# Optimization experiments

Hardware: AMD Instinct MI355X
Metric: run time of the kernel (lower is better)

Reference implementation:

```python
import jax, jax.numpy as jnp
import numpy as np

N_NODES = 100000
DIM = 64
N_EDGES = 1250000
NR_LAYERS = 1
EPS = 1e-12  # F.normalize default eps


def setup_inputs() -> dict:
    key = jax.random.key(0)
    k1, k2, k3 = jax.random.split(key, 3)
    x = jax.random.normal(k1, (N_NODES, DIM), dtype=jnp.float32)
    edge_index = jax.random.randint(k2, (2, N_EDGES), 0, N_NODES, dtype=jnp.int64 if jax.config.jax_enable_x64 else jnp.int32)
    edge_weights = jax.random.uniform(k3, (N_EDGES, 1), dtype=jnp.float32)
    return {"x": x, "edge_index": edge_index, "edge_weights": edge_weights}


def _scatter_mean(x, src, dst, n_nodes):
    # gather source features along edges, mean-reduce onto destination nodes
    sums = jax.ops.segment_sum(x[src], dst, num_segments=n_nodes)  # [N, D]
    cnt = jax.ops.segment_sum(jnp.ones((src.shape[0],), x.dtype), dst, num_segments=n_nodes)
    return sums / jnp.maximum(cnt, 1.0)[:, None]


def _layer(x, src, dst):
    # Faithful to source: update() overwrites the linear output with
    # F.normalize(aggr_out); out_f == out_b since new_edge_index == edge_index.
    agg = _scatter_mean(x, src, dst, x.shape[0])  # [N, D]
    norm = jnp.linalg.norm(agg, axis=1, keepdims=True)
    h = agg / jnp.maximum(norm, EPS)
    return 2.0 * h  # out_f + out_b


def reference(x, edge_index, edge_weights):
    src = edge_index[0]
    dst = edge_index[1]
    for _ in range(NR_LAYERS):
        x = _layer(x, src, dst)
        x = jax.nn.relu(x)
    return x
```

## Files before the change

kernel.cpp:

```cpp
#include <hip/hip_runtime.h>

#define N_NODES 100000
#define DIM 64
#define N_EDGES 1250000
#define EPS 1e-12f

#define PART 128
#define NP ((N_NODES + PART - 1) / PART)
#define SLOT 2048
#define CSTRIDE 16
#define CH 4096
#define NCH ((N_EDGES + CH - 1) / CH)
#define BT 1024
#define EPT (CH / BT)

typedef unsigned short ushort8 __attribute__((ext_vector_type(8)));

__device__ inline unsigned short f2bf(float f) {
    unsigned int u = __float_as_uint(f);
    return (unsigned short)((u + 0x7FFFu + ((u >> 16) & 1u)) >> 16);
}
__device__ inline float bf2f(unsigned short h) {
    return __uint_as_float(((unsigned int)h) << 16);
}

__global__ void convert_kernel(const float4* __restrict__ x4,
                               ushort8* __restrict__ xh8) {
    int i = blockIdx.x * blockDim.x + threadIdx.x;
    if (i < N_NODES * DIM / 8) {
        float4 a = x4[2 * i];
        float4 b = x4[2 * i + 1];
        ushort8 o;
        o[0] = f2bf(a.x); o[1] = f2bf(a.y); o[2] = f2bf(a.z); o[3] = f2bf(a.w);
        o[4] = f2bf(b.x); o[5] = f2bf(b.y); o[6] = f2bf(b.z); o[7] = f2bf(b.w);
        xh8[i] = o;
    }
}

__global__ __launch_bounds__(BT)
void bucket_kernel(const int* __restrict__ src,
                   const int* __restrict__ dst,
                   int* __restrict__ pcursor,
                   int* __restrict__ ebuf) {
    __shared__ int hist[NP];
    __shared__ int lstart[NP];
    __shared__ int cur[NP];
    __shared__ int gb[NP];
    __shared__ int sorted[CH];
    int t = threadIdx.x;
    int e0 = blockIdx.x * CH;

    for (int p = t; p < NP; p += BT) hist[p] = 0;
    __syncthreads();

    int d[EPT];
    #pragma unroll
    for (int i = 0; i < EPT; ++i) {
        int e = e0 + i * BT + t;
        d[i] = (e < N_EDGES) ? dst[e] : -1;
        if (d[i] >= 0) atomicAdd(&hist[d[i] >> 7], 1);
    }
    __syncthreads();

    for (int p = t; p < NP; p += BT) {
        int c = hist[p];
        gb[p] = c ? atomicAdd(&pcursor[p * CSTRIDE], c) : 0;
    }
    for (int p = t; p < NP; p += BT) cur[p] = hist[p];
    __syncthreads();
    for (int off = 1; off < NP; off <<= 1) {
        int v = 0;
        if (t < NP) { v = cur[t]; if (t >= off) v += cur[t - off]; }
        __syncthreads();
        if (t < NP) cur[t] = v;
        __syncthreads();
    }
    if (t < NP) lstart[t] = (t > 0) ? cur[t - 1] : 0;
    __syncthreads();
    if (t < NP) cur[t] = lstart[t];
    __syncthreads();

    #pragma unroll
    for (int i = 0; i < EPT; ++i) {
        if (d[i] >= 0) {
            int e = e0 + i * BT + t;
            int p = d[i] >> 7;
            int pos = atomicAdd(&cur[p], 1);
            sorted[pos] = (src[e] << 7) | (d[i] & 127);
        }
    }
    __syncthreads();

    int wave = t >> 6, lane = t & 63;
    for (int p = wave; p < NP; p += (BT / 64)) {
        int c = hist[p];
        int base = p * SLOT + gb[p];
        int ls = lstart[p];
        for (int off = lane; off < c; off += 64)
            ebuf[base + off] = sorted[ls + off];
    }
}

__global__ __launch_bounds__(1024, 8)
void aggregate_kernel(const ushort8* __restrict__ xh8,
                      const int* __restrict__ pcursor,
                      const int* __restrict__ ebuf,
                      float* __restrict__ out) {
    __shared__ int lraw[SLOT];
    __shared__ int lcsr[SLOT];
    __shared__ int lhist[PART];
    __shared__ int lcur[PART];
    int p = blockIdx.x;
    int t = threadIdx.x;
    int wave = t >> 6, lane = t & 63;
    int n = lane >> 3;
    int sub = lane & 7;

    if (t < PART) lhist[t] = 0;
    __syncthreads();

    int cnt = pcursor[p * CSTRIDE];
    const int* __restrict__ eb = ebuf + p * SLOT;
    for (int i = t; i < cnt; i += 1024) {
        int pk = eb[i];
        lraw[i] = pk;
        atomicAdd(&lhist[pk & 127], 1);
    }
    __syncthreads();

    for (int off = 1; off < PART; off <<= 1) {
        int v = 0;
        if (t < PART) { v = lhist[t]; if (t >= off) v += lhist[t - off]; }
        __syncthreads();
        if (t < PART) lhist[t] = v;
        __syncthreads();
    }
    if (t < PART) lcur[t] = (t > 0) ? lhist[t - 1] : 0;
    __syncthreads();

    for (int i = t; i < cnt; i += 1024) {
        int pk = lraw[i];
        int pos = atomicAdd(&lcur[pk & 127], 1);
        lcsr[pos] = pk >> 7;
    }
    __syncthreads();

    int nl = wave * 8 + n;
    int gnode = p * PART + nl;
    int beg = nl ? lhist[nl - 1] : 0;
    int dn  = lhist[nl] - beg;

    float acc[8] = {0.f,0.f,0.f,0.f,0.f,0.f,0.f,0.f};
    for (int e = 0; e < dn; e += 4) {
        #pragma unroll
        for (int i = 0; i < 4; ++i) {
            if (e + i < dn) {
                int s = lcsr[beg + e + i];
                ushort8 v = xh8[(size_t)s * 8 + sub];
                #pragma unroll
                for (int k = 0; k < 8; ++k) acc[k] += bf2f(v[k]);
            }
        }
    }

    float ss = 0.f;
    #pragma unroll
    for (int k = 0; k < 8; ++k) ss += acc[k] * acc[k];
    ss += __shfl_xor(ss, 1, 64);
    ss += __shfl_xor(ss, 2, 64);
    ss += __shfl_xor(ss, 4, 64);

    float scale = 2.0f / fmaxf(sqrtf(ss), EPS);
    if (gnode < N_NODES) {
        float4 o0, o1;
        o0.x = fmaxf(acc[0] * scale, 0.f); o0.y = fmaxf(acc[1] * scale, 0.f);
        o0.z = fmaxf(acc[2] * scale, 0.f); o0.w = fmaxf(acc[3] * scale, 0.f);
        o1.x = fmaxf(acc[4] * scale, 0.f); o1.y = fmaxf(acc[5] * scale, 0.f);
        o1.z = fmaxf(acc[6] * scale, 0.f); o1.w = fmaxf(acc[7] * scale, 0.f);
        ((float4*)out)[(size_t)gnode * 16 + 2 * sub]     = o0;
        ((float4*)out)[(size_t)gnode * 16 + 2 * sub + 1] = o1;
    }
}

extern "C" void kernel_launch(void* const* d_in, const int* in_sizes, int n_in,
                              void* d_out, int out_size, void* d_ws, size_t ws_size,
                              hipStream_t stream) {
    const float* x  = (const float*)d_in[0];
    const int*   ei = (const int*)d_in[1];
    float* out = (float*)d_out;

    const int* src = ei;
    const int* dst = ei + N_EDGES;

    ushort8* xh  = (ushort8*)d_ws;
    int* pcursor = (int*)((char*)d_ws + (size_t)N_NODES * DIM * 2);
    int* ebuf    = pcursor + NP * CSTRIDE;

    hipMemsetAsync(pcursor, 0, NP * CSTRIDE * sizeof(int), stream);

    int cvb = (N_NODES * DIM / 8 + 255) / 256;
    convert_kernel<<<cvb, 256, 0, stream>>>((const float4*)x, xh);

    bucket_kernel<<<NCH, BT, 0, stream>>>(src, dst, pcursor, ebuf);

    aggregate_kernel<<<NP, 1024, 0, stream>>>(xh, pcursor, ebuf, out);
}
```

Before: 150.3 us.

## Fuse convert into bucket kernel, use wave-shuffle scans, halve block size

Merges the bf16 conversion kernel and the edge-bucketing kernel into one launch, with extra blocks doing the conversion. Replaces the shared-memory Hillis-Steele scans, which needed many barriers, with wave-level shuffle scans in both kernels. Block size drops from 1024 to 512, so the aggregation kernel handles two node groups per thread. The bucket scatter becomes a flat per-edge loop that uses a stored partition id instead of a per-partition wave loop. This removes one launch and many barriers, at the cost of extra LDS for the partition-id array and less parallelism per block.

Result: faster. 132.8 us (-11.6%).

```diff
diff --git a/kernel.cpp b/kernel.cpp
--- a/kernel.cpp
+++ b/kernel.cpp
@@ -11,8 +11,9 @@
 #define CSTRIDE 16
 #define CH 4096
 #define NCH ((N_EDGES + CH - 1) / CH)
-#define BT 1024
+#define BT 512
 #define EPT (CH / BT)
+#define NCV ((N_NODES * DIM / 8 + BT - 1) / BT)
 
 typedef unsigned short ushort8 __attribute__((ext_vector_type(8)));
 
@@ -24,32 +25,37 @@
     return __uint_as_float(((unsigned int)h) << 16);
 }
 
-__global__ void convert_kernel(const float4* __restrict__ x4,
-                               ushort8* __restrict__ xh8) {
-    int i = blockIdx.x * blockDim.x + threadIdx.x;
-    if (i < N_NODES * DIM / 8) {
-        float4 a = x4[2 * i];
-        float4 b = x4[2 * i + 1];
-        ushort8 o;
-        o[0] = f2bf(a.x); o[1] = f2bf(a.y); o[2] = f2bf(a.z); o[3] = f2bf(a.w);
-        o[4] = f2bf(b.x); o[5] = f2bf(b.y); o[6] = f2bf(b.z); o[7] = f2bf(b.w);
-        xh8[i] = o;
-    }
-}
-
 __global__ __launch_bounds__(BT)
-void bucket_kernel(const int* __restrict__ src,
-                   const int* __restrict__ dst,
-                   int* __restrict__ pcursor,
-                   int* __restrict__ ebuf) {
+void convert_bucket_kernel(const float4* __restrict__ x4,
+                           ushort8* __restrict__ xh8,
+                           const int* __restrict__ src,
+                           const int* __restrict__ dst,
+                           int* __restrict__ pcursor,
+                           int* __restrict__ ebuf) {
     __shared__ int hist[NP];
     __shared__ int lstart[NP];
     __shared__ int cur[NP];
     __shared__ int gb[NP];
     __shared__ int sorted[CH];
+    __shared__ unsigned short pb[CH];
+    __shared__ int wsum[BT / 64];
+
     int t = threadIdx.x;
+
+    if (blockIdx.x >= NCH) {
+        int i = (blockIdx.x - NCH) * BT + t;
+        if (i < N_NODES * DIM / 8) {
+            float4 a = x4[2 * i];
+            float4 b = x4[2 * i + 1];
+            ushort8 o;
+            o[0] = f2bf(a.x); o[1] = f2bf(a.y); o[2] = f2bf(a.z); o[3] = f2bf(a.w);
+            o[4] = f2bf(b.x); o[5] = f2bf(b.y); o[6] = f2bf(b.z); o[7] = f2bf(b.w);
+            xh8[i] = o;
+        }
+        return;
+    }
+
     int e0 = blockIdx.x * CH;
-
     for (int p = t; p < NP; p += BT) hist[p] = 0;
     __syncthreads();
 
@@ -66,18 +72,29 @@
         int c = hist[p];
         gb[p] = c ? atomicAdd(&pcursor[p * CSTRIDE], c) : 0;
     }
-    for (int p = t; p < NP; p += BT) cur[p] = hist[p];
-    __syncthreads();
-    for (int off = 1; off < NP; off <<= 1) {
-        int v = 0;
-        if (t < NP) { v = cur[t]; if (t >= off) v += cur[t - off]; }
-        __syncthreads();
-        if (t < NP) cur[t] = v;
-        __syncthreads();
-    }
-    if (t < NP) lstart[t] = (t > 0) ? cur[t - 1] : 0;
-    __syncthreads();
-    if (t < NP) cur[t] = lstart[t];
+
+    int lane = t & 63, w = t >> 6;
+    int b0 = 2 * t, b1 = 2 * t + 1;
+    int c0 = (b0 < NP) ? hist[b0] : 0;
+    int c1 = (b1 < NP) ? hist[b1] : 0;
+    int ms = c0 + c1;
+    int v = ms;
+    #pragma unroll
+    for (int off = 1; off < 64; off <<= 1) {
+        int u = __shfl_up(v, off, 64);
+        if (lane >= off) v += u;
+    }
+    if (lane == 63) wsum[w] = v;
+    __syncthreads();
+    if (t == 0) {
+        int run = 0;
+        #pragma unroll
+        for (int i = 0; i < BT / 64; ++i) { int c = wsum[i]; wsum[i] = run; run += c; }
+    }
+    __syncthreads();
+    int excl = wsum[w] + v - ms;
+    if (b0 < NP) { lstart[b0] = excl;      cur[b0] = excl; }
+    if (b1 < NP) { lstart[b1] = excl + c0; cur[b1] = excl + c0; }
     __syncthreads();
 
     #pragma unroll
@@ -87,21 +104,20 @@
             int p = d[i] >> 7;
             int pos = atomicAdd(&cur[p], 1);
             sorted[pos] = (src[e] << 7) | (d[i] & 127);
-        }
-    }
-    __syncthreads();
-
-    int wave = t >> 6, lane = t & 63;
-    for (int p = wave; p < NP; p += (BT / 64)) {
-        int c = hist[p];
-        int base = p * SLOT + gb[p];
-        int ls = lstart[p];
-        for (int off = lane; off < c; off += 64)
-            ebuf[base + off] = sorted[ls + off];
-    }
-}
-
-__global__ __launch_bounds__(1024, 8)
+            pb[pos] = (unsigned short)p;
+        }
+    }
+    __syncthreads();
+
+    int vcnt = min(CH, N_EDGES - e0);
+    for (int i = t; i < vcnt; i += BT) {
+        int pk = sorted[i];
+        int p = pb[i];
+        ebuf[p * SLOT + gb[p] + (i - lstart[p])] = pk;
+    }
+}
+
+__global__ __launch_bounds__(BT, 8)
 void aggregate_kernel(const ushort8* __restrict__ xh8,
                       const int* __restrict__ pcursor,
                       const int* __restrict__ ebuf,
@@ -110,75 +126,87 @@
     __shared__ int lcsr[SLOT];
     __shared__ int lhist[PART];
     __shared__ int lcur[PART];
+    __shared__ int bridge;
     int p = blockIdx.x;
     int t = threadIdx.x;
-    int wave = t >> 6, lane = t & 63;
-    int n = lane >> 3;
-    int sub = lane & 7;
+    int lane = t & 63, w = t >> 6;
+    int n = lane >> 3, sub = lane & 7;
 
     if (t < PART) lhist[t] = 0;
     __syncthreads();
 
     int cnt = pcursor[p * CSTRIDE];
     const int* __restrict__ eb = ebuf + p * SLOT;
-    for (int i = t; i < cnt; i += 1024) {
+    for (int i = t; i < cnt; i += BT) {
         int pk = eb[i];
         lraw[i] = pk;
         atomicAdd(&lhist[pk & 127], 1);
     }
     __syncthreads();
 
-    for (int off = 1; off < PART; off <<= 1) {
-        int v = 0;
-        if (t < PART) { v = lhist[t]; if (t >= off) v += lhist[t - off]; }
-        __syncthreads();
-        if (t < PART) lhist[t] = v;
-        __syncthreads();
-    }
-    if (t < PART) lcur[t] = (t > 0) ? lhist[t - 1] : 0;
-    __syncthreads();
-
-    for (int i = t; i < cnt; i += 1024) {
+    int myc = 0, vincl = 0;
+    if (t < PART) {
+        myc = lhist[t];
+        vincl = myc;
+        #pragma unroll
+        for (int off = 1; off < 64; off <<= 1) {
+            int u = __shfl_up(vincl, off, 64);
+            if (lane >= off) vincl += u;
+        }
+        if (t == 63) bridge = vincl;
+    }
+    __syncthreads();
+    if (t < PART) {
+        int add = (t >= 64) ? bridge : 0;
+        lhist[t] = vincl + add;
+        lcur[t]  = vincl + add - myc;
+    }
+    __syncthreads();
+
+    for (int i = t; i < cnt; i += BT) {
         int pk = lraw[i];
         int pos = atomicAdd(&lcur[pk & 127], 1);
         lcsr[pos] = pk >> 7;
     }
     __syncthreads();
 
-    int nl = wave * 8 + n;
-    int gnode = p * PART + nl;
-    int beg = nl ? lhist[nl - 1] : 0;
-    int dn  = lhist[nl] - beg;
-
-    float acc[8] = {0.f,0.f,0.f,0.f,0.f,0.f,0.f,0.f};
-    for (int e = 0; e < dn; e += 4) {
+    #pragma unroll
+    for (int q = 0; q < 2; ++q) {
+        int nl = q * 64 + w * 8 + n;
+        int gnode = p * PART + nl;
+        int beg = nl ? lhist[nl - 1] : 0;
+        int dn  = lhist[nl] - beg;
+
+        float acc[8] = {0.f,0.f,0.f,0.f,0.f,0.f,0.f,0.f};
+        for (int e = 0; e < dn; e += 4) {
+            #pragma unroll
+            for (int i = 0; i < 4; ++i) {
+                if (e + i < dn) {
+                    int s = lcsr[beg + e + i];
+                    ushort8 vv = xh8[(size_t)s * 8 + sub];
+                    #pragma unroll
+                    for (int k = 0; k < 8; ++k) acc[k] += bf2f(vv[k]);
+                }
+            }
+        }
+
+        float ss = 0.f;
         #pragma unroll
-        for (int i = 0; i < 4; ++i) {
-            if (e + i < dn) {
-                int s = lcsr[beg + e + i];
-                ushort8 v = xh8[(size_t)s * 8 + sub];
-                #pragma unroll
-                for (int k = 0; k < 8; ++k) acc[k] += bf2f(v[k]);
-            }
-        }
-    }
-
-    float ss = 0.f;
-    #pragma unroll
-    for (int k = 0; k < 8; ++k) ss += acc[k] * acc[k];
-    ss += __shfl_xor(ss, 1, 64);
-    ss += __shfl_xor(ss, 2, 64);
-    ss += __shfl_xor(ss, 4, 64);
-
-    float scale = 2.0f / fmaxf(sqrtf(ss), EPS);
-    if (gnode < N_NODES) {
-        float4 o0, o1;
-        o0.x = fmaxf(acc[0] * scale, 0.f); o0.y = fmaxf(acc[1] * scale, 0.f);
-        o0.z = fmaxf(acc[2] * scale, 0.f); o0.w = fmaxf(acc[3] * scale, 0.f);
-        o1.x = fmaxf(acc[4] * scale, 0.f); o1.y = fmaxf(acc[5] * scale, 0.f);
-        o1.z = fmaxf(acc[6] * scale, 0.f); o1.w = fmaxf(acc[7] * scale, 0.f);
-        ((float4*)out)[(size_t)gnode * 16 + 2 * sub]     = o0;
-        ((float4*)out)[(size_t)gnode * 16 + 2 * sub + 1] = o1;
+        for (int k = 0; k < 8; ++k) ss += acc[k] * acc[k];
+        ss += __shfl_xor(ss, 1, 64);
+        ss += __shfl_xor(ss, 2, 64);
+        ss += __shfl_xor(ss, 4, 64);
+
+        float scale = 2.0f / fmaxf(sqrtf(ss), EPS);
+        if (gnode < N_NODES) {
+            float4 o0, o1;
+            o0.x = fmaxf(acc[0] * scale, 0.f); o0.y = fmaxf(acc[1] * scale, 0.f);
+            o0.z = fmaxf(acc[2] * scale, 0.f); o0.w = fmaxf(acc[3] * scale, 0.f);
+            o1.x = fmaxf(acc[4] * scale, 0.f); o1.y = fmaxf(acc[5] * scale, 0.f);
+            o1.z = fmaxf(acc[6] * scale, 0.f); o1.w = fmaxf(acc[7] * scale, 0.f);
+            ((float4*)out)[(size_t)gnode * 16 + 2 * sub]     = o0;
+            ((float4*)out)[(size_t)gnode * 16 + 2 * sub + 1] = o1;
+        }
     }
 }
 
@@ -198,10 +226,8 @@
 
     hipMemsetAsync(pcursor, 0, NP * CSTRIDE * sizeof(int), stream);
 
-    int cvb = (N_NODES * DIM / 8 + 255) / 256;
-    convert_kernel<<<cvb, 256, 0, stream>>>((const float4*)x, xh);
-
-    bucket_kernel<<<NCH, BT, 0, stream>>>(src, dst, pcursor, ebuf);
-
-    aggregate_kernel<<<NP, 1024, 0, stream>>>(xh, pcursor, ebuf, out);
-}
+    convert_bucket_kernel<<<NCH + NCV, BT, 0, stream>>>(
+        (const float4*)x, xh, src, dst, pcursor, ebuf);
+
+    aggregate_kernel<<<NP, BT, 0, stream>>>(xh, pcursor, ebuf, out);
+}
```
